# Performance work log

Hardware: AMD Instinct MI355X
Metric: run time of the kernel (lower is better)

The kernel has to match this reference:

```python
import jax, jax.numpy as jnp
import numpy as np

B, N, C, W = 128, 512, 128, 128
MASK_FILL = -1e-06  # faithful to original (sic: -1e-06, not -1e6)


def setup_inputs() -> dict:
    key = jax.random.key(0)
    ks = jax.random.split(key, 8)
    s = 1.0 / np.sqrt(C)
    return {
        "x": jax.random.normal(ks[0], (B, N, C), dtype=jnp.float32),
        "Wq": jax.random.normal(ks[1], (C, W), dtype=jnp.float32) * s,
        "bq": jnp.zeros((W,), dtype=jnp.float32),
        "Wk": jax.random.normal(ks[2], (C, W), dtype=jnp.float32) * s,
        "bk": jnp.zeros((W,), dtype=jnp.float32),
        "Wv": jax.random.normal(ks[3], (C, W), dtype=jnp.float32) * s,
        "bv": jnp.zeros((W,), dtype=jnp.float32),
        "valid_len": jax.random.randint(ks[4], (B,), 0, N, dtype=jnp.int64),
    }


def reference(x, Wq, bq, Wk, bk, Wv, bv, valid_len):
    # QKV projections: [B, N, W]
    q = jnp.einsum("bnc,cw->bnw", x, Wq) + bq
    k = jnp.einsum("bnc,cw->bnw", x, Wk) + bk
    v = jnp.einsum("bnc,cw->bnw", x, Wv) + bv
    # scores: [B, N, N]
    scores = jnp.einsum("bnw,bmw->bnm", q, k)
    # masked softmax: positions m where m > valid_len[b] get MASK_FILL
    # (mask is identical across query rows n since valid_len is per-batch)
    keep = jnp.arange(N)[None, None, :] <= valid_len[:, None, None]  # [B,1,N]
    scores = jnp.where(keep, scores, MASK_FILL)
    attn = jax.nn.softmax(scores, axis=-1)
    return jnp.einsum("bnm,bmw->bnw", attn, v)
```

## Files before the change

kernel.cpp:

```cpp
#include <hip/hip_runtime.h>
#include <hip/hip_fp16.h>
#include <math.h>

#define B_ 128
#define N_ 512
#define C_ 128
#define W_ 128
#define LDSW 136

typedef _Float16 f16;
typedef _Float16 f16x8 __attribute__((ext_vector_type(8)));
typedef _Float16 f16x4 __attribute__((ext_vector_type(4)));
typedef float f32x4 __attribute__((ext_vector_type(4)));

#define MFMA16(a, b, c) __builtin_amdgcn_mfma_f32_16x16x32_f16(a, b, c, 0, 0, 0)

#define LOG2E 1.44269504f
#define MASKF (-1e-6f * LOG2E)

__global__ __launch_bounds__(256) void prep_w(const float* __restrict__ Wq,
                                              const float* __restrict__ Wk,
                                              const float* __restrict__ Wv,
                                              f16* __restrict__ wT) {
  __shared__ float xs[16 * 129];
  const float* src = blockIdx.x == 0 ? Wq : (blockIdx.x == 1 ? Wk : Wv);
  f16* dst = wT + (size_t)blockIdx.x * C_ * W_;
  const int c0 = blockIdx.y * 16;
  const int t = threadIdx.x;
  for (int ii = 0; ii < 2; ++ii) {
    int idx = t + 256 * ii;
    int row = idx >> 5, w4 = idx & 31;
    float4 v = *reinterpret_cast<const float4*>(src + (c0 + row) * W_ + w4 * 4);
    xs[row * 129 + w4 * 4 + 0] = v.x;
    xs[row * 129 + w4 * 4 + 1] = v.y;
    xs[row * 129 + w4 * 4 + 2] = v.z;
    xs[row * 129 + w4 * 4 + 3] = v.w;
  }
  __syncthreads();
  int o = t * 8;
  int w = o >> 4, cc = o & 15;
  f16x8 h;
  for (int jj = 0; jj < 8; ++jj) h[jj] = (f16)xs[(cc + jj) * 129 + w];
  *reinterpret_cast<f16x8*>(dst + w * C_ + c0 + cc) = h;
}

__global__ __launch_bounds__(256, 2) void proj(const float* __restrict__ x,
                                               const float* __restrict__ bq,
                                               const float* __restrict__ bk,
                                               const float* __restrict__ bv,
                                               const f16* __restrict__ wT,
                                               f16* __restrict__ q,
                                               f16* __restrict__ k,
                                               f16* __restrict__ vT) {
  __shared__ f16 wls[2][128 * LDSW];
  const int b = blockIdx.y, n0 = blockIdx.x * 128;
  const int t = threadIdx.x, wave = t >> 6, lane = t & 63;
  const int quad = lane >> 4, l15 = lane & 15;

  float4 xr[2][4][2];
  for (int tile = 0; tile < 2; ++tile)
    for (int ks = 0; ks < 4; ++ks) {
      const float* p = x + ((size_t)(b * N_ + n0 + wave * 32 + tile * 16 +
                                     l15)) * C_ + ks * 32 + quad * 8;
      xr[tile][ks][0] = *reinterpret_cast<const float4*>(p);
      xr[tile][ks][1] = *reinterpret_cast<const float4*>(p + 4);
    }

  for (int i = 0; i < 8; ++i) {
    int idx = t + 256 * i;
    f16x8 tmp = *reinterpret_cast<const f16x8*>(wT + (size_t)idx * 8);
    *reinterpret_cast<f16x8*>(&wls[0][(idx >> 4) * LDSW + (idx & 15) * 8]) =
        tmp;
  }

  f16x8 af[2][4];
  for (int tile = 0; tile < 2; ++tile)
    for (int ks = 0; ks < 4; ++ks) {
      f16x8 h;
      h[0] = (f16)xr[tile][ks][0].x; h[1] = (f16)xr[tile][ks][0].y;
      h[2] = (f16)xr[tile][ks][0].z; h[3] = (f16)xr[tile][ks][0].w;
      h[4] = (f16)xr[tile][ks][1].x; h[5] = (f16)xr[tile][ks][1].y;
      h[6] = (f16)xr[tile][ks][1].z; h[7] = (f16)xr[tile][ks][1].w;
      af[tile][ks] = h;
    }
  __syncthreads();

  for (int ph = 0; ph < 3; ++ph) {
    const f16* wl = wls[ph & 1];

    f16x8 wst[8];
    if (ph < 2)
      for (int i = 0; i < 8; ++i)
        wst[i] = *reinterpret_cast<const f16x8*>(
            wT + (size_t)(ph + 1) * 16384 + (size_t)(t + 256 * i) * 8);

    f32x4 acc[8][2];
    for (int ct = 0; ct < 8; ++ct) {
      acc[ct][0] = {0.f, 0.f, 0.f, 0.f};
      acc[ct][1] = {0.f, 0.f, 0.f, 0.f};
    }

    if (ph < 2) {
      for (int ct = 0; ct < 8; ++ct) {
        f16x8 wf[4];
        for (int ks = 0; ks < 4; ++ks)
          wf[ks] = *reinterpret_cast<const f16x8*>(
              &wl[(ct * 16 + l15) * LDSW + ks * 32 + quad * 8]);
        for (int ks = 0; ks < 4; ++ks) {
          acc[ct][0] = MFMA16(wf[ks], af[0][ks], acc[ct][0]);
          acc[ct][1] = MFMA16(wf[ks], af[1][ks], acc[ct][1]);
        }
      }
      const float* bias = ph == 0 ? bq : bk;
      const float scale = ph == 0 ? LOG2E : 1.0f;
      f16* dst = ph == 0 ? q : k;
      for (int ct = 0; ct < 8; ++ct) {
        const float4 bb =
            *reinterpret_cast<const float4*>(bias + ct * 16 + quad * 4);
        for (int tile = 0; tile < 2; ++tile) {
          int n = n0 + wave * 32 + tile * 16 + l15;
          f16x4 h;
          h.x = (f16)((acc[ct][tile][0] + bb.x) * scale);
          h.y = (f16)((acc[ct][tile][1] + bb.y) * scale);
          h.z = (f16)((acc[ct][tile][2] + bb.z) * scale);
          h.w = (f16)((acc[ct][tile][3] + bb.w) * scale);
          *reinterpret_cast<f16x4*>(dst + ((size_t)(b * N_ + n)) * W_ +
                                    ct * 16 + quad * 4) = h;
        }
      }
    } else {
      for (int ct = 0; ct < 8; ++ct) {
        f16x8 wf[4];
        for (int ks = 0; ks < 4; ++ks)
          wf[ks] = *reinterpret_cast<const f16x8*>(
              &wl[(ct * 16 + l15) * LDSW + ks * 32 + quad * 8]);
        for (int ks = 0; ks < 4; ++ks) {
          acc[ct][0] = MFMA16(af[0][ks], wf[ks], acc[ct][0]);
          acc[ct][1] = MFMA16(af[1][ks], wf[ks], acc[ct][1]);
        }
      }
      for (int ct = 0; ct < 8; ++ct) {
        int wcol = ct * 16 + l15;
        float bb = bv[wcol];
        for (int tile = 0; tile < 2; ++tile) {
          int n = n0 + wave * 32 + tile * 16 + quad * 4;
          f16x4 h;
          h.x = (f16)(acc[ct][tile][0] + bb);
          h.y = (f16)(acc[ct][tile][1] + bb);
          h.z = (f16)(acc[ct][tile][2] + bb);
          h.w = (f16)(acc[ct][tile][3] + bb);
          *reinterpret_cast<f16x4*>(&vT[((size_t)(b * W_ + wcol)) * N_ + n]) =
              h;
        }
      }
    }

    if (ph < 2) {
      for (int i = 0; i < 8; ++i) {
        int idx = t + 256 * i;
        *reinterpret_cast<f16x8*>(
            &wls[(ph + 1) & 1][(idx >> 4) * LDSW + (idx & 15) * 8]) = wst[i];
      }
      __syncthreads();
    }
  }
}

__global__ __launch_bounds__(256, 2) void flash(const f16* __restrict__ q,
                                                const f16* __restrict__ k,
                                                const f16* __restrict__ vT,
                                                const int* __restrict__ vlen,
                                                float* __restrict__ out) {
  __shared__ f16 kls[128 * LDSW];
  __shared__ f16 pls[128 * LDSW];
  __shared__ float bcast[128];
  const int b = blockIdx.x, m0 = blockIdx.y * 128;
  const int t = threadIdx.x, wave = t >> 6, lane = t & 63;
  const int quad = lane >> 4, l15 = lane & 15;
  const int vl = vlen[b];
  const int mcol = m0 + wave * 32;
  const int srow = t >> 4, sc16 = t & 15;

  f16x8 qf[2][4];
  for (int ct = 0; ct < 2; ++ct)
    for (int kt = 0; kt < 4; ++kt)
      qf[ct][kt] = *reinterpret_cast<const f16x8*>(
          q + ((size_t)(b * N_ + mcol + ct * 16 + l15)) * W_ + kt * 32 +
          quad * 8);

  f32x4 oacc[2][8];
  for (int wt = 0; wt < 2; ++wt)
    for (int cm = 0; cm < 8; ++cm) oacc[wt][cm] = {0.f, 0.f, 0.f, 0.f};
  float mrun[2] = {-3.4e38f, -3.4e38f}, lrun[2] = {0.f, 0.f};

  for (int i = 0; i < 8; ++i) {
    int row = srow + 16 * i;
    f16x8 tmp = *reinterpret_cast<const f16x8*>(
        k + ((size_t)(b * N_ + row)) * W_ + sc16 * 8);
    *reinterpret_cast<f16x8*>(&kls[row * LDSW + sc16 * 8]) = tmp;
  }
  __syncthreads();

  for (int j = 0; j < 4; ++j) {
    const int n0 = j * 128;

    f16x8 vfa[4];
    for (int kt = 0; kt < 4; ++kt)
      vfa[kt] = *reinterpret_cast<const f16x8*>(
          vT + ((size_t)(b * W_ + wave * 32 + l15)) * N_ + n0 + kt * 32 +
          quad * 8);

    f16x8 kst[8];
    if (j < 3)
      for (int i = 0; i < 8; ++i)
        kst[i] = *reinterpret_cast<const f16x8*>(
            k + ((size_t)(b * N_ + n0 + 128 + srow + 16 * i)) * W_ + sc16 * 8);

    f32x4 sacc[8][2];
    for (int i = 0; i < 8; ++i) {
      sacc[i][0] = {0.f, 0.f, 0.f, 0.f};
      sacc[i][1] = {0.f, 0.f, 0.f, 0.f};
      f16x8 kf[4];
      for (int kt = 0; kt < 4; ++kt)
        kf[kt] = *reinterpret_cast<const f16x8*>(
            &kls[(i * 16 + l15) * LDSW + kt * 32 + quad * 8]);
      for (int kt = 0; kt < 4; ++kt) {
        sacc[i][0] = MFMA16(kf[kt], qf[0][kt], sacc[i][0]);
        sacc[i][1] = MFMA16(kf[kt], qf[1][kt], sacc[i][1]);
      }
    }

    for (int i = 0; i < 8; ++i)
      for (int r = 0; r < 4; ++r) {
        int n = n0 + 16 * i + quad * 4 + r;
        if (n > vl) { sacc[i][0][r] = MASKF; sacc[i][1][r] = MASKF; }
      }

    float alpha[2];
    for (int ct = 0; ct < 2; ++ct) {
      float mx = -3.4e38f;
      for (int i = 0; i < 8; ++i)
        for (int r = 0; r < 4; ++r) mx = fmaxf(mx, sacc[i][ct][r]);
      mx = fmaxf(mx, __shfl_xor(mx, 16));
      mx = fmaxf(mx, __shfl_xor(mx, 32));
      float mnew = fmaxf(mrun[ct], mx);
      alpha[ct] = exp2f(mrun[ct] - mnew);
      mrun[ct] = mnew;
      float s = 0.f;
      for (int i = 0; i < 8; ++i)
        for (int r = 0; r < 4; ++r) {
          float p = exp2f(sacc[i][ct][r] - mnew);
          sacc[i][ct][r] = p;
          s += p;
        }
      s += __shfl_xor(s, 16);
      s += __shfl_xor(s, 32);
      lrun[ct] = lrun[ct] * alpha[ct] + s;
    }

    for (int i = 0; i < 8; ++i)
      for (int ct = 0; ct < 2; ++ct) {
        f16x4 h;
        h.x = (f16)sacc[i][ct][0];
        h.y = (f16)sacc[i][ct][1];
        h.z = (f16)sacc[i][ct][2];
        h.w = (f16)sacc[i][ct][3];
        *reinterpret_cast<f16x4*>(
            &pls[(wave * 32 + ct * 16 + l15) * LDSW + 16 * i + quad * 4]) = h;
      }
    if (quad == 0) {
      bcast[wave * 32 + l15] = alpha[0];
      bcast[wave * 32 + 16 + l15] = alpha[1];
    }

    f16x8 vfb[4];
    for (int kt = 0; kt < 4; ++kt)
      vfb[kt] = *reinterpret_cast<const f16x8*>(
          vT + ((size_t)(b * W_ + wave * 32 + 16 + l15)) * N_ + n0 + kt * 32 +
          quad * 8);
    __syncthreads();

    if (j < 3)
      for (int i = 0; i < 8; ++i)
        *reinterpret_cast<f16x8*>(&kls[(srow + 16 * i) * LDSW + sc16 * 8]) =
            kst[i];

    float al[8];
    for (int cm = 0; cm < 8; ++cm) al[cm] = bcast[cm * 16 + l15];
    for (int wt = 0; wt < 2; ++wt)
      for (int cm = 0; cm < 8; ++cm) oacc[wt][cm] *= al[cm];
    for (int cm = 0; cm < 8; ++cm) {
      f16x8 pf[4];
      for (int kt = 0; kt < 4; ++kt)
        pf[kt] = *reinterpret_cast<const f16x8*>(
            &pls[(cm * 16 + l15) * LDSW + kt * 32 + quad * 8]);
      for (int kt = 0; kt < 4; ++kt) {
        oacc[0][cm] = MFMA16(vfa[kt], pf[kt], oacc[0][cm]);
        oacc[1][cm] = MFMA16(vfb[kt], pf[kt], oacc[1][cm]);
      }
    }
    __syncthreads();
  }

  if (quad == 0) {
    bcast[wave * 32 + l15] = 1.f / lrun[0];
    bcast[wave * 32 + 16 + l15] = 1.f / lrun[1];
  }
  __syncthreads();
  for (int cm = 0; cm < 8; ++cm) {
    float inv = bcast[cm * 16 + l15];
    int m = m0 + cm * 16 + l15;
    for (int wt = 0; wt < 2; ++wt) {
      int w = wave * 32 + wt * 16 + quad * 4;
      float4 o;
      o.x = oacc[wt][cm][0] * inv;
      o.y = oacc[wt][cm][1] * inv;
      o.z = oacc[wt][cm][2] * inv;
      o.w = oacc[wt][cm][3] * inv;
      *reinterpret_cast<float4*>(&out[((size_t)(b * N_ + m)) * W_ + w]) = o;
    }
  }
}

extern "C" void kernel_launch(void* const* d_in, const int* in_sizes, int n_in,
                              void* d_out, int out_size, void* d_ws,
                              size_t ws_size, hipStream_t stream) {
  const float* x  = (const float*)d_in[0];
  const float* Wq = (const float*)d_in[1];
  const float* bq = (const float*)d_in[2];
  const float* Wk = (const float*)d_in[3];
  const float* bk = (const float*)d_in[4];
  const float* Wv = (const float*)d_in[5];
  const float* bv = (const float*)d_in[6];
  const int* vlen = (const int*)d_in[7];
  float* out = (float*)d_out;

  char* ws = (char*)d_ws;
  f16* wT = (f16*)ws;
  f16* q  = (f16*)(ws + (1u << 20));
  f16* k  = (f16*)(ws + (1u << 20) + (16u << 20));
  f16* vT = (f16*)(ws + (1u << 20) + (32u << 20));

  prep_w<<<dim3(3, 8), 256, 0, stream>>>(Wq, Wk, Wv, wT);
  proj<<<dim3(4, 128), 256, 0, stream>>>(x, bq, bk, bv, wT, q, k, vT);
  flash<<<dim3(128, 4), 256, 0, stream>>>(q, k, vT, vlen, out);
}
```

Measured before the change: 140.7 us.

## Skip fully masked key chunks and fold masked tail into closed-form V sum

The flash kernel now loops only over 128-key chunks that contain unmasked positions. All masked keys share the same score (the mask fill value), so their contribution is added in closed form as a count times exp weight times the column sum of V over the tail. The proj kernel skips computing K for chunks entirely past valid_len. Flash also moves to 512 threads with 16 query rows per wave, which changes the occupancy and register balance, and the closed-form tail relies on every masked score being exactly equal.

After: 148.4 us. +5.4%, slower.

```diff
diff --git a/kernel.cpp b/kernel.cpp
--- a/kernel.cpp
+++ b/kernel.cpp
@@ -49,6 +49,7 @@
                                                const float* __restrict__ bk,
                                                const float* __restrict__ bv,
                                                const f16* __restrict__ wT,
+                                               const int* __restrict__ vlen,
                                                f16* __restrict__ q,
                                                f16* __restrict__ k,
                                                f16* __restrict__ vT) {
@@ -56,6 +57,8 @@
   const int b = blockIdx.y, n0 = blockIdx.x * 128;
   const int t = threadIdx.x, wave = t >> 6, lane = t & 63;
   const int quad = lane >> 4, l15 = lane & 15;
+  const int vl = vlen[b];
+  const bool doK = (n0 <= vl);
 
   float4 xr[2][4][2];
   for (int tile = 0; tile < 2; ++tile)
@@ -101,31 +104,33 @@
     }
 
     if (ph < 2) {
-      for (int ct = 0; ct < 8; ++ct) {
-        f16x8 wf[4];
-        for (int ks = 0; ks < 4; ++ks)
-          wf[ks] = *reinterpret_cast<const f16x8*>(
-              &wl[(ct * 16 + l15) * LDSW + ks * 32 + quad * 8]);
-        for (int ks = 0; ks < 4; ++ks) {
-          acc[ct][0] = MFMA16(wf[ks], af[0][ks], acc[ct][0]);
-          acc[ct][1] = MFMA16(wf[ks], af[1][ks], acc[ct][1]);
+      if (ph == 0 || doK) {
+        for (int ct = 0; ct < 8; ++ct) {
+          f16x8 wf[4];
+          for (int ks = 0; ks < 4; ++ks)
+            wf[ks] = *reinterpret_cast<const f16x8*>(
+                &wl[(ct * 16 + l15) * LDSW + ks * 32 + quad * 8]);
+          for (int ks = 0; ks < 4; ++ks) {
+            acc[ct][0] = MFMA16(wf[ks], af[0][ks], acc[ct][0]);
+            acc[ct][1] = MFMA16(wf[ks], af[1][ks], acc[ct][1]);
+          }
         }
-      }
-      const float* bias = ph == 0 ? bq : bk;
-      const float scale = ph == 0 ? LOG2E : 1.0f;
-      f16* dst = ph == 0 ? q : k;
-      for (int ct = 0; ct < 8; ++ct) {
-        const float4 bb =
-            *reinterpret_cast<const float4*>(bias + ct * 16 + quad * 4);
-        for (int tile = 0; tile < 2; ++tile) {
-          int n = n0 + wave * 32 + tile * 16 + l15;
-          f16x4 h;
-          h.x = (f16)((acc[ct][tile][0] + bb.x) * scale);
-          h.y = (f16)((acc[ct][tile][1] + bb.y) * scale);
-          h.z = (f16)((acc[ct][tile][2] + bb.z) * scale);
-          h.w = (f16)((acc[ct][tile][3] + bb.w) * scale);
-          *reinterpret_cast<f16x4*>(dst + ((size_t)(b * N_ + n)) * W_ +
-                                    ct * 16 + quad * 4) = h;
+        const float* bias = ph == 0 ? bq : bk;
+        const float scale = ph == 0 ? LOG2E : 1.0f;
+        f16* dst = ph == 0 ? q : k;
+        for (int ct = 0; ct < 8; ++ct) {
+          const float4 bb =
+              *reinterpret_cast<const float4*>(bias + ct * 16 + quad * 4);
+          for (int tile = 0; tile < 2; ++tile) {
+            int n = n0 + wave * 32 + tile * 16 + l15;
+            f16x4 h;
+            h.x = (f16)((acc[ct][tile][0] + bb.x) * scale);
+            h.y = (f16)((acc[ct][tile][1] + bb.y) * scale);
+            h.z = (f16)((acc[ct][tile][2] + bb.z) * scale);
+            h.w = (f16)((acc[ct][tile][3] + bb.w) * scale);
+            *reinterpret_cast<f16x4*>(dst + ((size_t)(b * N_ + n)) * W_ +
+                                      ct * 16 + quad * 4) = h;
+          }
         }
       }
     } else {
@@ -166,159 +171,171 @@
   }
 }
 
-__global__ __launch_bounds__(256, 2) void flash(const f16* __restrict__ q,
+__global__ __launch_bounds__(512, 2) void flash(const f16* __restrict__ q,
                                                 const f16* __restrict__ k,
                                                 const f16* __restrict__ vT,
                                                 const int* __restrict__ vlen,
                                                 float* __restrict__ out) {
-  __shared__ f16 kls[128 * LDSW];
-  __shared__ f16 pls[128 * LDSW];
+  __shared__ f16 kls[150 * LDSW];
+  __shared__ f16 pls[150 * LDSW];
   __shared__ float bcast[128];
+  __shared__ float vpart[512];
+  __shared__ float vsum[128];
   const int b = blockIdx.x, m0 = blockIdx.y * 128;
   const int t = threadIdx.x, wave = t >> 6, lane = t & 63;
   const int quad = lane >> 4, l15 = lane & 15;
   const int vl = vlen[b];
-  const int mcol = m0 + wave * 32;
+  const int nch = (vl >> 7) + 1;
+  const int ntail0 = nch << 7;
+  const int tailcnt = N_ - ntail0;
+  const int mcol = m0 + wave * 16;
   const int srow = t >> 4, sc16 = t & 15;
 
-  f16x8 qf[2][4];
-  for (int ct = 0; ct < 2; ++ct)
+  f16x8 qf[4];
+  for (int kt = 0; kt < 4; ++kt)
+    qf[kt] = *reinterpret_cast<const f16x8*>(
+        q + ((size_t)(b * N_ + mcol + l15)) * W_ + kt * 32 + quad * 8);
+
+  f32x4 oacc[8];
+  for (int cm = 0; cm < 8; ++cm) oacc[cm] = {0.f, 0.f, 0.f, 0.f};
+  float mrun = -3.4e38f, lrun = 0.f;
+
+  for (int i = 0; i < 4; ++i) {
+    int row = srow + 32 * i;
+    *reinterpret_cast<f16x8*>(&kls[row * LDSW + sc16 * 8]) =
+        *reinterpret_cast<const f16x8*>(k + ((size_t)(b * N_ + row)) * W_ +
+                                        sc16 * 8);
+  }
+  if (tailcnt > 0) {
+    int w = t & 127, g = t >> 7;
+    int cnt = tailcnt >> 2;
+    const f16* vp = vT + ((size_t)(b * W_ + w)) * N_ + ntail0 + g * cnt;
+    float s = 0.f;
+    for (int i = 0; i < cnt; i += 8) {
+      f16x8 h = *reinterpret_cast<const f16x8*>(vp + i);
+      for (int jj = 0; jj < 8; ++jj) s += (float)h[jj];
+    }
+    vpart[g * 128 + w] = s;
+  }
+  __syncthreads();
+  if (tailcnt > 0 && t < 128)
+    vsum[t] = vpart[t] + vpart[128 + t] + vpart[256 + t] + vpart[384 + t];
+
+  for (int j = 0; j < nch; ++j) {
+    const int n0 = j << 7;
+
+    f16x8 vf[4];
     for (int kt = 0; kt < 4; ++kt)
-      qf[ct][kt] = *reinterpret_cast<const f16x8*>(
-          q + ((size_t)(b * N_ + mcol + ct * 16 + l15)) * W_ + kt * 32 +
+      vf[kt] = *reinterpret_cast<const f16x8*>(
+          vT + ((size_t)(b * W_ + wave * 16 + l15)) * N_ + n0 + kt * 32 +
           quad * 8);
 
-  f32x4 oacc[2][8];
-  for (int wt = 0; wt < 2; ++wt)
-    for (int cm = 0; cm < 8; ++cm) oacc[wt][cm] = {0.f, 0.f, 0.f, 0.f};
-  float mrun[2] = {-3.4e38f, -3.4e38f}, lrun[2] = {0.f, 0.f};
-
-  for (int i = 0; i < 8; ++i) {
-    int row = srow + 16 * i;
-    f16x8 tmp = *reinterpret_cast<const f16x8*>(
-        k + ((size_t)(b * N_ + row)) * W_ + sc16 * 8);
-    *reinterpret_cast<f16x8*>(&kls[row * LDSW + sc16 * 8]) = tmp;
-  }
-  __syncthreads();
-
-  for (int j = 0; j < 4; ++j) {
-    const int n0 = j * 128;
-
-    f16x8 vfa[4];
-    for (int kt = 0; kt < 4; ++kt)
-      vfa[kt] = *reinterpret_cast<const f16x8*>(
-          vT + ((size_t)(b * W_ + wave * 32 + l15)) * N_ + n0 + kt * 32 +
-          quad * 8);
-
-    f16x8 kst[8];
-    if (j < 3)
-      for (int i = 0; i < 8; ++i)
+    f16x8 kst[4];
+    if (j < nch - 1)
+      for (int i = 0; i < 4; ++i)
         kst[i] = *reinterpret_cast<const f16x8*>(
-            k + ((size_t)(b * N_ + n0 + 128 + srow + 16 * i)) * W_ + sc16 * 8);
-
-    f32x4 sacc[8][2];
+            k + ((size_t)(b * N_ + n0 + 128 + srow + 32 * i)) * W_ + sc16 * 8);
+
+    f32x4 sacc[8];
     for (int i = 0; i < 8; ++i) {
-      sacc[i][0] = {0.f, 0.f, 0.f, 0.f};
-      sacc[i][1] = {0.f, 0.f, 0.f, 0.f};
+      sacc[i] = {0.f, 0.f, 0.f, 0.f};
       f16x8 kf[4];
       for (int kt = 0; kt < 4; ++kt)
         kf[kt] = *reinterpret_cast<const f16x8*>(
             &kls[(i * 16 + l15) * LDSW + kt * 32 + quad * 8]);
-      for (int kt = 0; kt < 4; ++kt) {
-        sacc[i][0] = MFMA16(kf[kt], qf[0][kt], sacc[i][0]);
-        sacc[i][1] = MFMA16(kf[kt], qf[1][kt], sacc[i][1]);
-      }
+      for (int kt = 0; kt < 4; ++kt)
+        sacc[i] = MFMA16(kf[kt], qf[kt], sacc[i]);
     }
 
     for (int i = 0; i < 8; ++i)
       for (int r = 0; r < 4; ++r) {
         int n = n0 + 16 * i + quad * 4 + r;
-        if (n > vl) { sacc[i][0][r] = MASKF; sacc[i][1][r] = MASKF; }
-      }
-
-    float alpha[2];
-    for (int ct = 0; ct < 2; ++ct) {
-      float mx = -3.4e38f;
-      for (int i = 0; i < 8; ++i)
-        for (int r = 0; r < 4; ++r) mx = fmaxf(mx, sacc[i][ct][r]);
-      mx = fmaxf(mx, __shfl_xor(mx, 16));
-      mx = fmaxf(mx, __shfl_xor(mx, 32));
-      float mnew = fmaxf(mrun[ct], mx);
-      alpha[ct] = exp2f(mrun[ct] - mnew);
-      mrun[ct] = mnew;
-      float s = 0.f;
-      for (int i = 0; i < 8; ++i)
-        for (int r = 0; r < 4; ++r) {
-          float p = exp2f(sacc[i][ct][r] - mnew);
-          sacc[i][ct][r] = p;
-          s += p;
-        }
-      s += __shfl_xor(s, 16);
-      s += __shfl_xor(s, 32);
-      lrun[ct] = lrun[ct] * alpha[ct] + s;
-    }
-
+        if (n > vl) sacc[i][r] = MASKF;
+      }
+
+    float mx = -3.4e38f;
     for (int i = 0; i < 8; ++i)
-      for (int ct = 0; ct < 2; ++ct) {
-        f16x4 h;
-        h.x = (f16)sacc[i][ct][0];
-        h.y = (f16)sacc[i][ct][1];
-        h.z = (f16)sacc[i][ct][2];
-        h.w = (f16)sacc[i][ct][3];
-        *reinterpret_cast<f16x4*>(
-            &pls[(wave * 32 + ct * 16 + l15) * LDSW + 16 * i + quad * 4]) = h;
-      }
-    if (quad == 0) {
-      bcast[wave * 32 + l15] = alpha[0];
-      bcast[wave * 32 + 16 + l15] = alpha[1];
-    }
-
-    f16x8 vfb[4];
-    for (int kt = 0; kt < 4; ++kt)
-      vfb[kt] = *reinterpret_cast<const f16x8*>(
-          vT + ((size_t)(b * W_ + wave * 32 + 16 + l15)) * N_ + n0 + kt * 32 +
-          quad * 8);
+      for (int r = 0; r < 4; ++r) mx = fmaxf(mx, sacc[i][r]);
+    mx = fmaxf(mx, __shfl_xor(mx, 16));
+    mx = fmaxf(mx, __shfl_xor(mx, 32));
+    float mnew = fmaxf(mrun, mx);
+    float alpha = exp2f(mrun - mnew);
+    mrun = mnew;
+    float s = 0.f;
+    for (int i = 0; i < 8; ++i)
+      for (int r = 0; r < 4; ++r) {
+        float p = exp2f(sacc[i][r] - mnew);
+        sacc[i][r] = p;
+        s += p;
+      }
+    s += __shfl_xor(s, 16);
+    s += __shfl_xor(s, 32);
+    lrun = lrun * alpha + s;
+
+    for (int i = 0; i < 8; ++i) {
+      f16x4 h;
+      h.x = (f16)sacc[i][0];
+      h.y = (f16)sacc[i][1];
+      h.z = (f16)sacc[i][2];
+      h.w = (f16)sacc[i][3];
+      *reinterpret_cast<f16x4*>(
+          &pls[(wave * 16 + l15) * LDSW + 16 * i + quad * 4]) = h;
+    }
+    if (quad == 0) bcast[wave * 16 + l15] = alpha;
     __syncthreads();
 
-    if (j < 3)
-      for (int i = 0; i < 8; ++i)
-        *reinterpret_cast<f16x8*>(&kls[(srow + 16 * i) * LDSW + sc16 * 8]) =
+    if (j < nch - 1)
+      for (int i = 0; i < 4; ++i)
+        *reinterpret_cast<f16x8*>(&kls[(srow + 32 * i) * LDSW + sc16 * 8]) =
             kst[i];
 
     float al[8];
     for (int cm = 0; cm < 8; ++cm) al[cm] = bcast[cm * 16 + l15];
-    for (int wt = 0; wt < 2; ++wt)
-      for (int cm = 0; cm < 8; ++cm) oacc[wt][cm] *= al[cm];
+    for (int cm = 0; cm < 8; ++cm) oacc[cm] *= al[cm];
     for (int cm = 0; cm < 8; ++cm) {
       f16x8 pf[4];
       for (int kt = 0; kt < 4; ++kt)
         pf[kt] = *reinterpret_cast<const f16x8*>(
             &pls[(cm * 16 + l15) * LDSW + kt * 32 + quad * 8]);
-      for (int kt = 0; kt < 4; ++kt) {
-        oacc[0][cm] = MFMA16(vfa[kt], pf[kt], oacc[0][cm]);
-        oacc[1][cm] = MFMA16(vfb[kt], pf[kt], oacc[1][cm]);
-      }
+      for (int kt = 0; kt < 4; ++kt)
+        oacc[cm] = MFMA16(vf[kt], pf[kt], oacc[cm]);
     }
     __syncthreads();
   }
 
-  if (quad == 0) {
-    bcast[wave * 32 + l15] = 1.f / lrun[0];
-    bcast[wave * 32 + 16 + l15] = 1.f / lrun[1];
-  }
+  if (tailcnt > 0) {
+    float mfin = fmaxf(mrun, MASKF);
+    float at = exp2f(mrun - mfin);
+    float pm = exp2f(MASKF - mfin);
+    lrun = lrun * at + (float)tailcnt * pm;
+    if (quad == 0) {
+      vpart[wave * 16 + l15] = at;
+      vpart[128 + wave * 16 + l15] = pm;
+    }
+  }
+  if (quad == 0) bcast[wave * 16 + l15] = 1.f / lrun;
   __syncthreads();
+
+  if (tailcnt > 0) {
+    const int w0 = wave * 16 + quad * 4;
+    for (int cm = 0; cm < 8; ++cm) {
+      float at = vpart[cm * 16 + l15];
+      float pm = vpart[128 + cm * 16 + l15];
+      for (int r = 0; r < 4; ++r)
+        oacc[cm][r] = oacc[cm][r] * at + pm * vsum[w0 + r];
+    }
+  }
+
   for (int cm = 0; cm < 8; ++cm) {
     float inv = bcast[cm * 16 + l15];
     int m = m0 + cm * 16 + l15;
-    for (int wt = 0; wt < 2; ++wt) {
-      int w = wave * 32 + wt * 16 + quad * 4;
-      float4 o;
-      o.x = oacc[wt][cm][0] * inv;
-      o.y = oacc[wt][cm][1] * inv;
-      o.z = oacc[wt][cm][2] * inv;
-      o.w = oacc[wt][cm][3] * inv;
-      *reinterpret_cast<float4*>(&out[((size_t)(b * N_ + m)) * W_ + w]) = o;
-    }
+    int w = wave * 16 + quad * 4;
+    float4 o;
+    o.x = oacc[cm][0] * inv;
+    o.y = oacc[cm][1] * inv;
+    o.z = oacc[cm][2] * inv;
+    o.w = oacc[cm][3] * inv;
+    *reinterpret_cast<float4*>(&out[((size_t)(b * N_ + m)) * W_ + w]) = o;
   }
 }
 
@@ -342,6 +359,6 @@
   f16* vT = (f16*)(ws + (1u << 20) + (32u << 20));
 
   prep_w<<<dim3(3, 8), 256, 0, stream>>>(Wq, Wk, Wv, wT);
-  proj<<<dim3(4, 128), 256, 0, stream>>>(x, bq, bk, bv, wT, q, k, vT);
-  flash<<<dim3(128, 4), 256, 0, stream>>>(q, k, vT, vlen, out);
+  proj<<<dim3(4, 128), 256, 0, stream>>>(x, bq, bk, bv, wT, vlen, q, k, vT);
+  flash<<<dim3(128, 4), 512, 0, stream>>>(q, k, vT, vlen, out);
 }
```

## Skip fully masked key chunks and fold their contribution in via precomputed V sums

Applied to the files above, without the earlier changes.

Masked keys all carry the same constant score, so their softmax contribution equals a single weight times the sum of the masked V rows. The projection kernel now skips K/V stores for fully masked 128-row chunks and atomically accumulates per-batch V column sums for them instead. The flash kernel iterates only over unmasked chunks and adds the tail analytically. It also pulls work items from an atomic counter over a list sorted longest-first, to balance the now variable per-item cost. This adds atomics, an extra prep pass and a persistent-loop structure, and the reordered accumulation can change rounding slightly.

Measured after the change: 153.3 us. 1.09x slower.

```diff
diff --git a/kernel.cpp b/kernel.cpp
--- a/kernel.cpp
+++ b/kernel.cpp
@@ -21,12 +21,49 @@
 __global__ __launch_bounds__(256) void prep_w(const float* __restrict__ Wq,
                                               const float* __restrict__ Wk,
                                               const float* __restrict__ Wv,
-                                              f16* __restrict__ wT) {
+                                              const int* __restrict__ vlen,
+                                              f16* __restrict__ wT,
+                                              int* __restrict__ wlist,
+                                              int* __restrict__ ctr,
+                                              float* __restrict__ Vsuf) {
+  const int t = threadIdx.x;
+  if (blockIdx.y == 8) {
+    if (blockIdx.x == 0) {
+      __shared__ int cnt[5];
+      __shared__ int off[5];
+      __shared__ int nchs[128];
+      if (t < 5) cnt[t] = 0;
+      __syncthreads();
+      if (t < 128) {
+        int nch = (vlen[t] >> 7) + 1;
+        nchs[t] = nch;
+        atomicAdd(&cnt[nch], 1);
+      }
+      __syncthreads();
+      if (t == 0) {
+        off[4] = 0;
+        off[3] = cnt[4] * 4;
+        off[2] = (cnt[4] + cnt[3]) * 4;
+        off[1] = (cnt[4] + cnt[3] + cnt[2]) * 4;
+        *ctr = 0;
+      }
+      __syncthreads();
+      if (t < 128) {
+        int base = atomicAdd(&off[nchs[t]], 4);
+        for (int mt = 0; mt < 4; ++mt) wlist[base + mt] = (t << 2) | mt;
+      }
+    } else if (blockIdx.x == 1) {
+      for (int i = 0; i < 16; ++i) {
+        float4 z = {0.f, 0.f, 0.f, 0.f};
+        *reinterpret_cast<float4*>(Vsuf + (size_t)(t + 256 * i) * 4) = z;
+      }
+    }
+    return;
+  }
   __shared__ float xs[16 * 129];
   const float* src = blockIdx.x == 0 ? Wq : (blockIdx.x == 1 ? Wk : Wv);
   f16* dst = wT + (size_t)blockIdx.x * C_ * W_;
   const int c0 = blockIdx.y * 16;
-  const int t = threadIdx.x;
   for (int ii = 0; ii < 2; ++ii) {
     int idx = t + 256 * ii;
     int row = idx >> 5, w4 = idx & 31;
@@ -49,13 +86,17 @@
                                                const float* __restrict__ bk,
                                                const float* __restrict__ bv,
                                                const f16* __restrict__ wT,
+                                               const int* __restrict__ vlen,
                                                f16* __restrict__ q,
                                                f16* __restrict__ k,
-                                               f16* __restrict__ vT) {
+                                               f16* __restrict__ vT,
+                                               float* __restrict__ Vsuf) {
   __shared__ f16 wls[2][128 * LDSW];
   const int b = blockIdx.y, n0 = blockIdx.x * 128;
   const int t = threadIdx.x, wave = t >> 6, lane = t & 63;
   const int quad = lane >> 4, l15 = lane & 15;
+  const int vl = vlen[b];
+  const bool fullmask = (n0 > vl);
 
   float4 xr[2][4][2];
   for (int tile = 0; tile < 2; ++tile)
@@ -101,31 +142,33 @@
     }
 
     if (ph < 2) {
-      for (int ct = 0; ct < 8; ++ct) {
-        f16x8 wf[4];
-        for (int ks = 0; ks < 4; ++ks)
-          wf[ks] = *reinterpret_cast<const f16x8*>(
-              &wl[(ct * 16 + l15) * LDSW + ks * 32 + quad * 8]);
-        for (int ks = 0; ks < 4; ++ks) {
-          acc[ct][0] = MFMA16(wf[ks], af[0][ks], acc[ct][0]);
-          acc[ct][1] = MFMA16(wf[ks], af[1][ks], acc[ct][1]);
-        }
-      }
-      const float* bias = ph == 0 ? bq : bk;
-      const float scale = ph == 0 ? LOG2E : 1.0f;
-      f16* dst = ph == 0 ? q : k;
-      for (int ct = 0; ct < 8; ++ct) {
-        const float4 bb =
-            *reinterpret_cast<const float4*>(bias + ct * 16 + quad * 4);
-        for (int tile = 0; tile < 2; ++tile) {
-          int n = n0 + wave * 32 + tile * 16 + l15;
-          f16x4 h;
-          h.x = (f16)((acc[ct][tile][0] + bb.x) * scale);
-          h.y = (f16)((acc[ct][tile][1] + bb.y) * scale);
-          h.z = (f16)((acc[ct][tile][2] + bb.z) * scale);
-          h.w = (f16)((acc[ct][tile][3] + bb.w) * scale);
-          *reinterpret_cast<f16x4*>(dst + ((size_t)(b * N_ + n)) * W_ +
-                                    ct * 16 + quad * 4) = h;
+      if (ph == 0 || !fullmask) {
+        for (int ct = 0; ct < 8; ++ct) {
+          f16x8 wf[4];
+          for (int ks = 0; ks < 4; ++ks)
+            wf[ks] = *reinterpret_cast<const f16x8*>(
+                &wl[(ct * 16 + l15) * LDSW + ks * 32 + quad * 8]);
+          for (int ks = 0; ks < 4; ++ks) {
+            acc[ct][0] = MFMA16(wf[ks], af[0][ks], acc[ct][0]);
+            acc[ct][1] = MFMA16(wf[ks], af[1][ks], acc[ct][1]);
+          }
+        }
+        const float* bias = ph == 0 ? bq : bk;
+        const float scale = ph == 0 ? LOG2E : 1.0f;
+        f16* dst = ph == 0 ? q : k;
+        for (int ct = 0; ct < 8; ++ct) {
+          const float4 bb =
+              *reinterpret_cast<const float4*>(bias + ct * 16 + quad * 4);
+          for (int tile = 0; tile < 2; ++tile) {
+            int n = n0 + wave * 32 + tile * 16 + l15;
+            f16x4 h;
+            h.x = (f16)((acc[ct][tile][0] + bb.x) * scale);
+            h.y = (f16)((acc[ct][tile][1] + bb.y) * scale);
+            h.z = (f16)((acc[ct][tile][2] + bb.z) * scale);
+            h.w = (f16)((acc[ct][tile][3] + bb.w) * scale);
+            *reinterpret_cast<f16x4*>(dst + ((size_t)(b * N_ + n)) * W_ +
+                                      ct * 16 + quad * 4) = h;
+          }
         }
       }
     } else {
@@ -142,15 +185,24 @@
       for (int ct = 0; ct < 8; ++ct) {
         int wcol = ct * 16 + l15;
         float bb = bv[wcol];
-        for (int tile = 0; tile < 2; ++tile) {
-          int n = n0 + wave * 32 + tile * 16 + quad * 4;
-          f16x4 h;
-          h.x = (f16)(acc[ct][tile][0] + bb);
-          h.y = (f16)(acc[ct][tile][1] + bb);
-          h.z = (f16)(acc[ct][tile][2] + bb);
-          h.w = (f16)(acc[ct][tile][3] + bb);
-          *reinterpret_cast<f16x4*>(&vT[((size_t)(b * W_ + wcol)) * N_ + n]) =
-              h;
+        if (!fullmask) {
+          for (int tile = 0; tile < 2; ++tile) {
+            int n = n0 + wave * 32 + tile * 16 + quad * 4;
+            f16x4 h;
+            h.x = (f16)(acc[ct][tile][0] + bb);
+            h.y = (f16)(acc[ct][tile][1] + bb);
+            h.z = (f16)(acc[ct][tile][2] + bb);
+            h.w = (f16)(acc[ct][tile][3] + bb);
+            *reinterpret_cast<f16x4*>(&vT[((size_t)(b * W_ + wcol)) * N_ + n]) =
+                h;
+          }
+        } else {
+          float s = 0.f;
+          for (int tile = 0; tile < 2; ++tile)
+            for (int r = 0; r < 4; ++r) s += acc[ct][tile][r] + bb;
+          s += __shfl_xor(s, 16);
+          s += __shfl_xor(s, 32);
+          if (quad == 0) atomicAdd(&Vsuf[b * 128 + wcol], s);
         }
       }
     }
@@ -170,154 +222,201 @@
                                                 const f16* __restrict__ k,
                                                 const f16* __restrict__ vT,
                                                 const int* __restrict__ vlen,
+                                                const float* __restrict__ Vsuf,
+                                                const int* __restrict__ wlist,
+                                                int* __restrict__ ctr,
                                                 float* __restrict__ out) {
   __shared__ f16 kls[128 * LDSW];
   __shared__ f16 pls[128 * LDSW];
   __shared__ float bcast[128];
-  const int b = blockIdx.x, m0 = blockIdx.y * 128;
+  __shared__ int s_slot;
   const int t = threadIdx.x, wave = t >> 6, lane = t & 63;
   const int quad = lane >> 4, l15 = lane & 15;
-  const int vl = vlen[b];
-  const int mcol = m0 + wave * 32;
   const int srow = t >> 4, sc16 = t & 15;
 
-  f16x8 qf[2][4];
-  for (int ct = 0; ct < 2; ++ct)
-    for (int kt = 0; kt < 4; ++kt)
-      qf[ct][kt] = *reinterpret_cast<const f16x8*>(
-          q + ((size_t)(b * N_ + mcol + ct * 16 + l15)) * W_ + kt * 32 +
-          quad * 8);
-
-  f32x4 oacc[2][8];
-  for (int wt = 0; wt < 2; ++wt)
-    for (int cm = 0; cm < 8; ++cm) oacc[wt][cm] = {0.f, 0.f, 0.f, 0.f};
-  float mrun[2] = {-3.4e38f, -3.4e38f}, lrun[2] = {0.f, 0.f};
-
-  for (int i = 0; i < 8; ++i) {
-    int row = srow + 16 * i;
-    f16x8 tmp = *reinterpret_cast<const f16x8*>(
-        k + ((size_t)(b * N_ + row)) * W_ + sc16 * 8);
-    *reinterpret_cast<f16x8*>(&kls[row * LDSW + sc16 * 8]) = tmp;
-  }
-  __syncthreads();
-
-  for (int j = 0; j < 4; ++j) {
-    const int n0 = j * 128;
-
-    f16x8 vfa[4];
-    for (int kt = 0; kt < 4; ++kt)
-      vfa[kt] = *reinterpret_cast<const f16x8*>(
-          vT + ((size_t)(b * W_ + wave * 32 + l15)) * N_ + n0 + kt * 32 +
-          quad * 8);
-
-    f16x8 kst[8];
-    if (j < 3)
+  while (true) {
+    if (t == 0) s_slot = atomicAdd(ctr, 1);
+    __syncthreads();
+    const int slot = s_slot;
+    if (slot >= 512) break;
+    const int item = wlist[slot];
+    const int b = item >> 2, m0 = (item & 3) << 7;
+    const int vl = vlen[b];
+    const int nch = (vl >> 7) + 1;
+    const int tailcnt = N_ - (nch << 7);
+    const int mcol = m0 + wave * 32;
+
+    f16x8 qf[2][4];
+    for (int ct = 0; ct < 2; ++ct)
+      for (int kt = 0; kt < 4; ++kt)
+        qf[ct][kt] = *reinterpret_cast<const f16x8*>(
+            q + ((size_t)(b * N_ + mcol + ct * 16 + l15)) * W_ + kt * 32 +
+            quad * 8);
+
+    f32x4 oacc[2][8];
+    for (int wt = 0; wt < 2; ++wt)
+      for (int cm = 0; cm < 8; ++cm) oacc[wt][cm] = {0.f, 0.f, 0.f, 0.f};
+    float mrun[2] = {-3.4e38f, -3.4e38f}, lrun[2] = {0.f, 0.f};
+
+    for (int i = 0; i < 8; ++i) {
+      int row = srow + 16 * i;
+      f16x8 tmp = *reinterpret_cast<const f16x8*>(
+          k + ((size_t)(b * N_ + row)) * W_ + sc16 * 8);
+      *reinterpret_cast<f16x8*>(&kls[row * LDSW + sc16 * 8]) = tmp;
+    }
+    __syncthreads();
+
+    for (int j = 0; j < nch; ++j) {
+      const int n0 = j << 7;
+
+      f16x8 vfa[4];
+      for (int kt = 0; kt < 4; ++kt)
+        vfa[kt] = *reinterpret_cast<const f16x8*>(
+            vT + ((size_t)(b * W_ + wave * 32 + l15)) * N_ + n0 + kt * 32 +
+            quad * 8);
+
+      f16x8 kst[8];
+      if (j < nch - 1)
+        for (int i = 0; i < 8; ++i)
+          kst[i] = *reinterpret_cast<const f16x8*>(
+              k + ((size_t)(b * N_ + n0 + 128 + srow + 16 * i)) * W_ +
+              sc16 * 8);
+
+      f32x4 sacc[8][2];
+      for (int i = 0; i < 8; ++i) {
+        sacc[i][0] = {0.f, 0.f, 0.f, 0.f};
+        sacc[i][1] = {0.f, 0.f, 0.f, 0.f};
+        f16x8 kf[4];
+        for (int kt = 0; kt < 4; ++kt)
+          kf[kt] = *reinterpret_cast<const f16x8*>(
+              &kls[(i * 16 + l15) * LDSW + kt * 32 + quad * 8]);
+        for (int kt = 0; kt < 4; ++kt) {
+          sacc[i][0] = MFMA16(kf[kt], qf[0][kt], sacc[i][0]);
+          sacc[i][1] = MFMA16(kf[kt], qf[1][kt], sacc[i][1]);
+        }
+      }
+
+      if (j == nch - 1 && vl < (nch << 7) - 1) {
+        for (int i = 0; i < 8; ++i)
+          for (int r = 0; r < 4; ++r) {
+            int n = n0 + 16 * i + quad * 4 + r;
+            if (n > vl) { sacc[i][0][r] = MASKF; sacc[i][1][r] = MASKF; }
+          }
+      }
+
+      float alpha[2];
+      for (int ct = 0; ct < 2; ++ct) {
+        float mx = -3.4e38f;
+        for (int i = 0; i < 8; ++i)
+          for (int r = 0; r < 4; ++r) mx = fmaxf(mx, sacc[i][ct][r]);
+        mx = fmaxf(mx, __shfl_xor(mx, 16));
+        mx = fmaxf(mx, __shfl_xor(mx, 32));
+        float mnew = fmaxf(mrun[ct], mx);
+        alpha[ct] = exp2f(mrun[ct] - mnew);
+        mrun[ct] = mnew;
+        float s = 0.f;
+        for (int i = 0; i < 8; ++i)
+          for (int r = 0; r < 4; ++r) {
+            float p = exp2f(sacc[i][ct][r] - mnew);
+            sacc[i][ct][r] = p;
+            s += p;
+          }
+        s += __shfl_xor(s, 16);
+        s += __shfl_xor(s, 32);
+        lrun[ct] = lrun[ct] * alpha[ct] + s;
+      }
+
       for (int i = 0; i < 8; ++i)
-        kst[i] = *reinterpret_cast<const f16x8*>(
-            k + ((size_t)(b * N_ + n0 + 128 + srow + 16 * i)) * W_ + sc16 * 8);
-
-    f32x4 sacc[8][2];
-    for (int i = 0; i < 8; ++i) {
-      sacc[i][0] = {0.f, 0.f, 0.f, 0.f};
-      sacc[i][1] = {0.f, 0.f, 0.f, 0.f};
-      f16x8 kf[4];
+        for (int ct = 0; ct < 2; ++ct) {
+          f16x4 h;
+          h.x = (f16)sacc[i][ct][0];
+          h.y = (f16)sacc[i][ct][1];
+          h.z = (f16)sacc[i][ct][2];
+          h.w = (f16)sacc[i][ct][3];
+          *reinterpret_cast<f16x4*>(
+              &pls[(wave * 32 + ct * 16 + l15) * LDSW + 16 * i + quad * 4]) =
+              h;
+        }
+      if (quad == 0) {
+        bcast[wave * 32 + l15] = alpha[0];
+        bcast[wave * 32 + 16 + l15] = alpha[1];
+      }
+
+      f16x8 vfb[4];
       for (int kt = 0; kt < 4; ++kt)
-        kf[kt] = *reinterpret_cast<const f16x8*>(
-            &kls[(i * 16 + l15) * LDSW + kt * 32 + quad * 8]);
-      for (int kt = 0; kt < 4; ++kt) {
-        sacc[i][0] = MFMA16(kf[kt], qf[0][kt], sacc[i][0]);
-        sacc[i][1] = MFMA16(kf[kt], qf[1][kt], sacc[i][1]);
-      }
-    }
-
-    for (int i = 0; i < 8; ++i)
-      for (int r = 0; r < 4; ++r) {
-        int n = n0 + 16 * i + quad * 4 + r;
-        if (n > vl) { sacc[i][0][r] = MASKF; sacc[i][1][r] = MASKF; }
-      }
-
-    float alpha[2];
-    for (int ct = 0; ct < 2; ++ct) {
-      float mx = -3.4e38f;
-      for (int i = 0; i < 8; ++i)
-        for (int r = 0; r < 4; ++r) mx = fmaxf(mx, sacc[i][ct][r]);
-      mx = fmaxf(mx, __shfl_xor(mx, 16));
-      mx = fmaxf(mx, __shfl_xor(mx, 32));
-      float mnew = fmaxf(mrun[ct], mx);
-      alpha[ct] = exp2f(mrun[ct] - mnew);
-      mrun[ct] = mnew;
-      float s = 0.f;
-      for (int i = 0; i < 8; ++i)
-        for (int r = 0; r < 4; ++r) {
-          float p = exp2f(sacc[i][ct][r] - mnew);
-          sacc[i][ct][r] = p;
-          s += p;
-        }
-      s += __shfl_xor(s, 16);
-      s += __shfl_xor(s, 32);
-      lrun[ct] = lrun[ct] * alpha[ct] + s;
-    }
-
-    for (int i = 0; i < 8; ++i)
+        vfb[kt] = *reinterpret_cast<const f16x8*>(
+            vT + ((size_t)(b * W_ + wave * 32 + 16 + l15)) * N_ + n0 +
+            kt * 32 + quad * 8);
+      __syncthreads();
+
+      if (j < nch - 1)
+        for (int i = 0; i < 8; ++i)
+          *reinterpret_cast<f16x8*>(&kls[(srow + 16 * i) * LDSW + sc16 * 8]) =
+              kst[i];
+
+      float al[8];
+      for (int cm = 0; cm < 8; ++cm) al[cm] = bcast[cm * 16 + l15];
+      for (int wt = 0; wt < 2; ++wt)
+        for (int cm = 0; cm < 8; ++cm) oacc[wt][cm] *= al[cm];
+      for (int cm = 0; cm < 8; ++cm) {
+        f16x8 pf[4];
+        for (int kt = 0; kt < 4; ++kt)
+          pf[kt] = *reinterpret_cast<const f16x8*>(
+              &pls[(cm * 16 + l15) * LDSW + kt * 32 + quad * 8]);
+        for (int kt = 0; kt < 4; ++kt) {
+          oacc[0][cm] = MFMA16(vfa[kt], pf[kt], oacc[0][cm]);
+          oacc[1][cm] = MFMA16(vfb[kt], pf[kt], oacc[1][cm]);
+        }
+      }
+      __syncthreads();
+    }
+
+    float* fb = reinterpret_cast<float*>(pls);
+    if (tailcnt > 0) {
       for (int ct = 0; ct < 2; ++ct) {
-        f16x4 h;
-        h.x = (f16)sacc[i][ct][0];
-        h.y = (f16)sacc[i][ct][1];
-        h.z = (f16)sacc[i][ct][2];
-        h.w = (f16)sacc[i][ct][3];
-        *reinterpret_cast<f16x4*>(
-            &pls[(wave * 32 + ct * 16 + l15) * LDSW + 16 * i + quad * 4]) = h;
-      }
+        float mfin = fmaxf(mrun[ct], MASKF);
+        float at = exp2f(mrun[ct] - mfin);
+        float pm = exp2f(MASKF - mfin);
+        lrun[ct] = lrun[ct] * at + (float)tailcnt * pm;
+        if (quad == 0) {
+          fb[wave * 32 + ct * 16 + l15] = at;
+          fb[128 + wave * 32 + ct * 16 + l15] = pm;
+        }
+      }
+    }
     if (quad == 0) {
-      bcast[wave * 32 + l15] = alpha[0];
-      bcast[wave * 32 + 16 + l15] = alpha[1];
-    }
-
-    f16x8 vfb[4];
-    for (int kt = 0; kt < 4; ++kt)
-      vfb[kt] = *reinterpret_cast<const f16x8*>(
-          vT + ((size_t)(b * W_ + wave * 32 + 16 + l15)) * N_ + n0 + kt * 32 +
-          quad * 8);
+      bcast[wave * 32 + l15] = 1.f / lrun[0];
+      bcast[wave * 32 + 16 + l15] = 1.f / lrun[1];
+    }
     __syncthreads();
 
-    if (j < 3)
-      for (int i = 0; i < 8; ++i)
-        *reinterpret_cast<f16x8*>(&kls[(srow + 16 * i) * LDSW + sc16 * 8]) =
-            kst[i];
-
-    float al[8];
-    for (int cm = 0; cm < 8; ++cm) al[cm] = bcast[cm * 16 + l15];
-    for (int wt = 0; wt < 2; ++wt)
-      for (int cm = 0; cm < 8; ++cm) oacc[wt][cm] *= al[cm];
+    if (tailcnt > 0) {
+      float4 vs[2];
+      vs[0] = *reinterpret_cast<const float4*>(Vsuf + b * 128 + wave * 32 +
+                                               quad * 4);
+      vs[1] = *reinterpret_cast<const float4*>(Vsuf + b * 128 + wave * 32 +
+                                               16 + quad * 4);
+      for (int cm = 0; cm < 8; ++cm) {
+        float at = fb[cm * 16 + l15];
+        float pm = fb[128 + cm * 16 + l15];
+        for (int wt = 0; wt < 2; ++wt)
+          for (int r = 0; r < 4; ++r)
+            oacc[wt][cm][r] = oacc[wt][cm][r] * at + pm * vs[wt][r];
+      }
+    }
+
     for (int cm = 0; cm < 8; ++cm) {
-      f16x8 pf[4];
-      for (int kt = 0; kt < 4; ++kt)
-        pf[kt] = *reinterpret_cast<const f16x8*>(
-            &pls[(cm * 16 + l15) * LDSW + kt * 32 + quad * 8]);
-      for (int kt = 0; kt < 4; ++kt) {
-        oacc[0][cm] = MFMA16(vfa[kt], pf[kt], oacc[0][cm]);
-        oacc[1][cm] = MFMA16(vfb[kt], pf[kt], oacc[1][cm]);
-      }
-    }
-    __syncthreads();
-  }
-
-  if (quad == 0) {
-    bcast[wave * 32 + l15] = 1.f / lrun[0];
-    bcast[wave * 32 + 16 + l15] = 1.f / lrun[1];
-  }
-  __syncthreads();
-  for (int cm = 0; cm < 8; ++cm) {
-    float inv = bcast[cm * 16 + l15];
-    int m = m0 + cm * 16 + l15;
-    for (int wt = 0; wt < 2; ++wt) {
-      int w = wave * 32 + wt * 16 + quad * 4;
-      float4 o;
-      o.x = oacc[wt][cm][0] * inv;
-      o.y = oacc[wt][cm][1] * inv;
-      o.z = oacc[wt][cm][2] * inv;
-      o.w = oacc[wt][cm][3] * inv;
-      *reinterpret_cast<float4*>(&out[((size_t)(b * N_ + m)) * W_ + w]) = o;
+      float inv = bcast[cm * 16 + l15];
+      int m = m0 + cm * 16 + l15;
+      for (int wt = 0; wt < 2; ++wt) {
+        int w = wave * 32 + wt * 16 + quad * 4;
+        float4 o;
+        o.x = oacc[wt][cm][0] * inv;
+        o.y = oacc[wt][cm][1] * inv;
+        o.z = oacc[wt][cm][2] * inv;
+        o.w = oacc[wt][cm][3] * inv;
+        *reinterpret_cast<float4*>(&out[((size_t)(b * N_ + m)) * W_ + w]) = o;
+      }
     }
   }
 }
@@ -336,12 +435,18 @@
   float* out = (float*)d_out;
 
   char* ws = (char*)d_ws;
-  f16* wT = (f16*)ws;
+  f16* wT     = (f16*)ws;
+  int* wlist  = (int*)(ws + (128u << 10));
+  int* ctr    = (int*)(ws + (132u << 10));
+  float* Vsuf = (float*)(ws + (192u << 10));
   f16* q  = (f16*)(ws + (1u << 20));
   f16* k  = (f16*)(ws + (1u << 20) + (16u << 20));
   f16* vT = (f16*)(ws + (1u << 20) + (32u << 20));
 
-  prep_w<<<dim3(3, 8), 256, 0, stream>>>(Wq, Wk, Wv, wT);
-  proj<<<dim3(4, 128), 256, 0, stream>>>(x, bq, bk, bv, wT, q, k, vT);
-  flash<<<dim3(128, 4), 256, 0, stream>>>(q, k, vT, vlen, out);
+  prep_w<<<dim3(3, 9), 256, 0, stream>>>(Wq, Wk, Wv, vlen, wT, wlist, ctr,
+                                         Vsuf);
+  proj<<<dim3(4, 128), 256, 0, stream>>>(x, bq, bk, bv, wT, vlen, q, k, vT,
+                                         Vsuf);
+  flash<<<dim3(512, 1), 256, 0, stream>>>(q, k, vT, vlen, Vsuf, wlist, ctr,
+                                          out);
 }
```
